# Performance work log

Measured on AMD Instinct MI355X. Metric: run time of the kernel, lower is better.

Reference implementation:

```python
import jax, jax.numpy as jnp
import numpy as np

N_NODES = 100000
N_EDGES = 1600000
IN_DIM = 64
HID = 128
N_GRAPHS = 64
N_CLASSES = 2
EPS = 1e-5


def setup_inputs() -> dict:
    key = jax.random.key(0)
    ks = jax.random.split(key, 8)
    x = jax.random.normal(ks[0], (N_NODES, IN_DIM), dtype=jnp.float32)
    edge_index = jax.random.randint(ks[1], (2, N_EDGES), 0, N_NODES, dtype=jnp.int64)
    batch = jnp.sort(jax.random.randint(ks[2], (N_NODES,), 0, N_GRAPHS, dtype=jnp.int64))
    W1 = jax.random.normal(ks[3], (IN_DIM, HID), dtype=jnp.float32) / np.sqrt(IN_DIM)
    b1 = jnp.zeros((HID,), jnp.float32)
    W2 = jax.random.normal(ks[4], (HID, HID), dtype=jnp.float32) / np.sqrt(HID)
    b2 = jnp.zeros((HID,), jnp.float32)
    gamma = jnp.ones((HID,), jnp.float32)
    beta = jnp.zeros((HID,), jnp.float32)
    fcW = jax.random.normal(ks[5], (HID, N_CLASSES), dtype=jnp.float32) / np.sqrt(HID)
    fcb = jnp.zeros((N_CLASSES,), jnp.float32)
    return {"x": x, "edge_index": edge_index, "batch": batch, "W1": W1, "b1": b1,
            "W2": W2, "b2": b2, "gamma": gamma, "beta": beta, "fcW": fcW, "fcb": fcb}


def reference(x, edge_index, batch, W1, b1, W2, b2, gamma, beta, fcW, fcb):
    n = x.shape[0]
    loop = jnp.arange(n)
    # GCNConv adds self-loops and uses symmetric normalization D^-1/2 (A+I) D^-1/2
    src = jnp.concatenate([edge_index[0], loop])
    dst = jnp.concatenate([edge_index[1], loop])
    deg = jax.ops.segment_sum(jnp.ones_like(dst, dtype=x.dtype), dst, num_segments=n)
    dis = jax.lax.rsqrt(deg)  # deg >= 1 thanks to self-loops
    enorm = dis[src] * dis[dst]  # [E+N]

    def gcn(h, W, b):
        h = h @ W                                   # transform first (PyG order)
        msg = h[src] * enorm[:, None]               # gather + scale
        return jax.ops.segment_sum(msg, dst, num_segments=n) + b  # scatter-add

    cnt = jnp.maximum(jax.ops.segment_sum(jnp.ones((n,), x.dtype), batch,
                                          num_segments=N_GRAPHS), 1.0)[:, None]

    def inst_norm(h):
        # per-graph, per-channel normalization over nodes (affine=False)
        mean = jax.ops.segment_sum(h, batch, num_segments=N_GRAPHS) / cnt
        var = jax.ops.segment_sum(h * h, batch, num_segments=N_GRAPHS) / cnt - mean * mean
        return (h - mean[batch]) * jax.lax.rsqrt(var[batch] + EPS)

    h = jax.nn.relu(inst_norm(gcn(x, W1, b1)))   # dropout = identity (eval)
    h = jax.nn.relu(inst_norm(gcn(h, W2, b2)))
    pooled = jax.ops.segment_sum(h, batch, num_segments=N_GRAPHS) / cnt  # global mean pool
    # BatchNorm1d over the graph dimension (batch statistics, affine)
    m = jnp.mean(pooled, axis=0)
    v = jnp.mean((pooled - m) ** 2, axis=0)
    z = (pooled - m) * jax.lax.rsqrt(v + EPS) * gamma + beta
    return z @ fcW + fcb
```

## Files before the change

### kernel.cpp

```cpp
#include <hip/hip_runtime.h>
#include <hip/hip_bf16.h>


#define HID 128
#define NGRAPH 64
#define EPSN 1e-5f
#define BSHIFT 8
#define NBMAX 512

typedef unsigned int uint;
typedef unsigned short ushort;

static __device__ __forceinline__ ushort f2bf(float f) {
  uint x = __float_as_uint(f);
  return (ushort)((x + 0x7FFFu + ((x >> 16) & 1u)) >> 16);
}
static __device__ __forceinline__ float bf_lo(uint u) { return __uint_as_float(u << 16); }
static __device__ __forceinline__ float bf_hi(uint u) {
  return __uint_as_float(u & 0xFFFF0000u);
}

__global__ __launch_bounds__(256) void graph_starts(const int* __restrict__ batch,
                                                    int* __restrict__ gstart, int N) {
  int i = blockIdx.x * 256 + threadIdx.x;
  if (i >= N) return;
  int g = batch[i];
  if (i == 0) {
    for (int q = 0; q <= g; ++q) gstart[q] = 0;
  } else {
    int gp = batch[i - 1];
    if (g != gp)
      for (int q = gp + 1; q <= g; ++q) gstart[q] = i;
  }
  if (i == N - 1)
    for (int q = g + 1; q <= NGRAPH; ++q) gstart[q] = N;
}

__global__ __launch_bounds__(64) void cnt_from_starts(const int* __restrict__ gstart,
                                                      float* __restrict__ cnt) {
  int g = threadIdx.x;
  if (g < NGRAPH) cnt[g] = (float)(gstart[g + 1] - gstart[g]);
}

__global__ __launch_bounds__(256) void bucket_count(const int* __restrict__ dst,
                                                    int* __restrict__ bcnt, int E, int NB) {
  __shared__ int h[NBMAX];
  for (int i = threadIdx.x; i < NB; i += 256) h[i] = 0;
  __syncthreads();
  int e0 = blockIdx.x * 4096;
#pragma unroll
  for (int k = 0; k < 16; ++k) {
    int e = e0 + k * 256 + threadIdx.x;
    if (e < E) atomicAdd(&h[dst[e] >> BSHIFT], 1);
  }
  __syncthreads();
  for (int i = threadIdx.x; i < NB; i += 256)
    if (h[i]) atomicAdd(&bcnt[i], h[i]);
}

__global__ __launch_bounds__(512) void bucket_scan(const int* __restrict__ bcnt,
                                                   int* __restrict__ bbase,
                                                   int* __restrict__ bcursor, int NB, int E) {
  __shared__ int sm[512];
  int t = threadIdx.x;
  int v = (t < NB) ? bcnt[t] : 0;
  sm[t] = v;
  __syncthreads();
  for (int off = 1; off < 512; off <<= 1) {
    int add = (t >= off) ? sm[t - off] : 0;
    __syncthreads();
    sm[t] += add;
    __syncthreads();
  }
  if (t < NB) {
    int excl = sm[t] - v;
    bbase[t] = excl;
    bcursor[t] = excl;
  }
  if (t == 0) bbase[NB] = E;
}

__global__ __launch_bounds__(256) void bin_edges(const int* __restrict__ src,
                                                 const int* __restrict__ dst,
                                                 int* __restrict__ bcursor,
                                                 uint* __restrict__ records, int E, int NB) {
  __shared__ int h[NBMAX];
  __shared__ int base[NBMAX];
  for (int i = threadIdx.x; i < NB; i += 256) h[i] = 0;
  __syncthreads();
  int e0 = blockIdx.x * 4096;
  int d[16], s[16];
#pragma unroll
  for (int k = 0; k < 16; ++k) {
    int e = e0 + k * 256 + threadIdx.x;
    if (e < E) {
      d[k] = dst[e];
      s[k] = src[e];
      atomicAdd(&h[d[k] >> BSHIFT], 1);
    }
  }
  __syncthreads();
  for (int i = threadIdx.x; i < NB; i += 256) {
    int c = h[i];
    if (c) base[i] = atomicAdd(&bcursor[i], c);
  }
  __syncthreads();
  for (int i = threadIdx.x; i < NB; i += 256) h[i] = 0;
  __syncthreads();
#pragma unroll
  for (int k = 0; k < 16; ++k) {
    int e = e0 + k * 256 + threadIdx.x;
    if (e < E) {
      int b = d[k] >> BSHIFT;
      int lp = atomicAdd(&h[b], 1);
      records[base[b] + lp] = ((uint)s[k] << 8) | (uint)(d[k] & 255);
    }
  }
}

__global__ __launch_bounds__(256) void build_csr(const uint* __restrict__ records,
                                                 const int* __restrict__ bbase,
                                                 int* __restrict__ row_ptr,
                                                 float* __restrict__ dis,
                                                 int* __restrict__ esrc, int N, int E) {
  const int b = blockIdx.x;
  const int node0 = b << BSHIFT;
  const int nn = min(256, N - node0);
  const int beg = bbase[b];
  const int cnt = bbase[b + 1] - beg;
  const int t = threadIdx.x;
  __shared__ int lc[256], sc[256], lcur[256];
  lc[t] = 0;
  __syncthreads();
  for (int i = t; i < cnt; i += 256) atomicAdd(&lc[records[beg + i] & 255u], 1);
  __syncthreads();
  int myc = lc[t];
  sc[t] = myc;
  __syncthreads();
  for (int off = 1; off < 256; off <<= 1) {
    int add = (t >= off) ? sc[t - off] : 0;
    __syncthreads();
    sc[t] += add;
    __syncthreads();
  }
  int excl = sc[t] - myc;
  if (t < nn) {
    row_ptr[node0 + t] = beg + excl;
    dis[node0 + t] = rsqrtf((float)myc + 1.0f);
  }
  lcur[t] = excl;
  __syncthreads();
  for (int i = t; i < cnt; i += 256) {
    uint r = records[beg + i];
    int p = atomicAdd(&lcur[r & 255u], 1);
    esrc[beg + p] = (int)(r >> 8);
  }
  if (b == 0 && t == 0) row_ptr[N] = E;
}

__global__ __launch_bounds__(256) void xscale_bf16(const float* __restrict__ X,
                                                   const float* __restrict__ dis,
                                                   ushort* __restrict__ XS, int n4) {
  int i4 = blockIdx.x * 256 + threadIdx.x;
  if (i4 >= n4) return;
  int n = i4 >> 4;
  float dn = dis[n];
  float4 v = ((const float4*)X)[i4];
  ushort4 u;
  u.x = f2bf(v.x * dn);
  u.y = f2bf(v.y * dn);
  u.z = f2bf(v.z * dn);
  u.w = f2bf(v.w * dn);
  ((ushort4*)XS)[i4] = u;
}

__global__ __launch_bounds__(256) void aggregate64_bf16(const ushort* __restrict__ XS,
                                                        const int* __restrict__ row_ptr,
                                                        const int* __restrict__ esrc,
                                                        const float* __restrict__ dis,
                                                        ushort* __restrict__ out, int N) {
  int wid = (int)((blockIdx.x * 256 + threadIdx.x) >> 6);
  if (wid >= N) return;
  const int lane = threadIdx.x & 63;
  const int h = lane >> 5;
  const int c2 = lane & 31;
  const float dn = dis[wid];
  const int beg = row_ptr[wid];
  const int end = row_ptr[wid + 1];
  const uint* X32 = (const uint*)XS;
  float ax = 0.f, ay = 0.f, bx = 0.f, by = 0.f;
  int e = beg;
  for (; e + 3 < end; e += 4) {
    int s0 = esrc[e + h];
    int s1 = esrc[e + 2 + h];
    uint u0 = X32[(size_t)s0 * 32 + c2];
    uint u1 = X32[(size_t)s1 * 32 + c2];
    ax += bf_lo(u0);
    ay += bf_hi(u0);
    bx += bf_lo(u1);
    by += bf_hi(u1);
  }
  for (; e < end; e += 2) {
    if (e + h < end) {
      uint u0 = X32[(size_t)esrc[e + h] * 32 + c2];
      ax += bf_lo(u0);
      ay += bf_hi(u0);
    }
  }
  ax += bx;
  ay += by;
  ax += __shfl_xor(ax, 32, 64);
  ay += __shfl_xor(ay, 32, 64);
  if (h == 0) {
    uint us = X32[(size_t)wid * 32 + c2];
    ax = (ax + bf_lo(us)) * dn;
    ay = (ay + bf_hi(us)) * dn;
    ((uint*)out)[(size_t)wid * 32 + c2] = (uint)f2bf(ax) | ((uint)f2bf(ay) << 16);
  }
}

__global__ __launch_bounds__(256) void aggregate128_bf16(const ushort* __restrict__ H,
                                                         const int* __restrict__ row_ptr,
                                                         const int* __restrict__ esrc,
                                                         const float* __restrict__ dis,
                                                         const float* __restrict__ bias,
                                                         ushort* __restrict__ outz, int N) {
  int wid = (int)((blockIdx.x * 256 + threadIdx.x) >> 6);
  if (wid >= N) return;
  const int lane = threadIdx.x & 63;
  const int h = lane >> 5;
  const int c4 = lane & 31;
  const float dn = dis[wid];
  const int beg = row_ptr[wid];
  const int end = row_ptr[wid + 1];
  const uint2* H2 = (const uint2*)H;
  float a0 = 0.f, a1 = 0.f, a2 = 0.f, a3 = 0.f;
  float b0 = 0.f, b1v = 0.f, b2v = 0.f, b3 = 0.f;
  int e = beg;
  for (; e + 3 < end; e += 4) {
    int s0 = esrc[e + h];
    int s1 = esrc[e + 2 + h];
    uint2 u0 = H2[(size_t)s0 * 32 + c4];
    uint2 u1 = H2[(size_t)s1 * 32 + c4];
    a0 += bf_lo(u0.x);
    a1 += bf_hi(u0.x);
    a2 += bf_lo(u0.y);
    a3 += bf_hi(u0.y);
    b0 += bf_lo(u1.x);
    b1v += bf_hi(u1.x);
    b2v += bf_lo(u1.y);
    b3 += bf_hi(u1.y);
  }
  for (; e < end; e += 2) {
    if (e + h < end) {
      uint2 u0 = H2[(size_t)esrc[e + h] * 32 + c4];
      a0 += bf_lo(u0.x);
      a1 += bf_hi(u0.x);
      a2 += bf_lo(u0.y);
      a3 += bf_hi(u0.y);
    }
  }
  a0 += b0;
  a1 += b1v;
  a2 += b2v;
  a3 += b3;
  a0 += __shfl_xor(a0, 32, 64);
  a1 += __shfl_xor(a1, 32, 64);
  a2 += __shfl_xor(a2, 32, 64);
  a3 += __shfl_xor(a3, 32, 64);
  if (h == 0) {
    uint2 us = H2[(size_t)wid * 32 + c4];
    float4 b = ((const float4*)bias)[c4];
    float r0 = (a0 + bf_lo(us.x)) * dn + b.x;
    float r1 = (a1 + bf_hi(us.x)) * dn + b.y;
    float r2 = (a2 + bf_lo(us.y)) * dn + b.z;
    float r3 = (a3 + bf_hi(us.y)) * dn + b.w;
    uint2 o;
    o.x = (uint)f2bf(r0) | ((uint)f2bf(r1) << 16);
    o.y = (uint)f2bf(r2) | ((uint)f2bf(r3) << 16);
    ((uint2*)outz)[(size_t)wid * 32 + c4] = o;
  }
}

template <int K, bool FUSE_NORM, bool DIS_SCALE>
__global__ __launch_bounds__(256) void gemm_tile(const ushort* __restrict__ X,
                                                 const float* __restrict__ W,
                                                 const float* __restrict__ bias,
                                                 const int* __restrict__ batch,
                                                 const float* __restrict__ mean,
                                                 const float* __restrict__ inv,
                                                 const float* __restrict__ disv,
                                                 ushort* __restrict__ Y, int N) {
  __shared__ float Xs[64][68];
  __shared__ float Ws[64][HID];
  const int t = threadIdx.x;
  const int r0 = (t >> 4) * 4;
  const int c0 = (t & 15) * 8;
  const int row0 = blockIdx.x * 64;
  float acc[4][8] = {};
  for (int k0 = 0; k0 < K; k0 += 64) {
    for (int i = t; i < 64 * 32; i += 256) {
      int kk = i >> 5;
      int c4 = i & 31;
      ((float4*)&Ws[kk][0])[c4] = ((const float4*)(W + (size_t)(k0 + kk) * HID))[c4];
    }
    for (int i = t; i < 64 * 8; i += 256) {
      int r = i >> 3;
      int u = i & 7;
      int gr = row0 + r;
      float f[8];
      if (gr < N) {
        uint4 v = *(const uint4*)(X + (size_t)gr * K + k0 + u * 8);
        f[0] = bf_lo(v.x);
        f[1] = bf_hi(v.x);
        f[2] = bf_lo(v.y);
        f[3] = bf_hi(v.y);
        f[4] = bf_lo(v.z);
        f[5] = bf_hi(v.z);
        f[6] = bf_lo(v.w);
        f[7] = bf_hi(v.w);
        if (FUSE_NORM) {
          int g = batch[gr];
          const float* mp = mean + g * HID + k0 + u * 8;
          const float* ip = inv + g * HID + k0 + u * 8;
#pragma unroll
          for (int j = 0; j < 8; ++j) f[j] = fmaxf((f[j] - mp[j]) * ip[j], 0.f);
        }
      } else {
#pragma unroll
        for (int j = 0; j < 8; ++j) f[j] = 0.f;
      }
#pragma unroll
      for (int j = 0; j < 8; ++j) Xs[r][u * 8 + j] = f[j];
    }
    __syncthreads();
#pragma unroll 4
    for (int kk = 0; kk < 64; ++kk) {
      float4 w0 = *(const float4*)&Ws[kk][c0];
      float4 w1 = *(const float4*)&Ws[kk][c0 + 4];
      float xr[4];
#pragma unroll
      for (int i = 0; i < 4; ++i) xr[i] = Xs[r0 + i][kk];
#pragma unroll
      for (int i = 0; i < 4; ++i) {
        acc[i][0] += xr[i] * w0.x;
        acc[i][1] += xr[i] * w0.y;
        acc[i][2] += xr[i] * w0.z;
        acc[i][3] += xr[i] * w0.w;
        acc[i][4] += xr[i] * w1.x;
        acc[i][5] += xr[i] * w1.y;
        acc[i][6] += xr[i] * w1.z;
        acc[i][7] += xr[i] * w1.w;
      }
    }
    __syncthreads();
  }
  float bv[8];
#pragma unroll
  for (int j = 0; j < 8; ++j) bv[j] = bias ? bias[c0 + j] : 0.f;
#pragma unroll
  for (int i = 0; i < 4; ++i) {
    int gr = row0 + r0 + i;
    if (gr < N) {
      float ds = DIS_SCALE ? disv[gr] : 1.f;
      uint4 u;
      u.x = (uint)f2bf((acc[i][0] + bv[0]) * ds) | ((uint)f2bf((acc[i][1] + bv[1]) * ds) << 16);
      u.y = (uint)f2bf((acc[i][2] + bv[2]) * ds) | ((uint)f2bf((acc[i][3] + bv[3]) * ds) << 16);
      u.z = (uint)f2bf((acc[i][4] + bv[4]) * ds) | ((uint)f2bf((acc[i][5] + bv[5]) * ds) << 16);
      u.w = (uint)f2bf((acc[i][6] + bv[6]) * ds) | ((uint)f2bf((acc[i][7] + bv[7]) * ds) << 16);
      *(uint4*)(Y + (size_t)gr * HID + c0) = u;
    }
  }
}

__global__ __launch_bounds__(256) void stats_pass(const ushort* __restrict__ G,
                                                  const int* __restrict__ batch,
                                                  float* __restrict__ gsum,
                                                  float* __restrict__ gsq, int N) {
  const int c = threadIdx.x & 127;
  const int half = threadIdx.x >> 7;
  const int n0 = blockIdx.x * 64 + half * 32;
  const int n1 = min(n0 + 32, N);
  float s = 0.f, sq = 0.f;
  int cur = -1;
  for (int n = n0; n < n1; ++n) {
    int g = batch[n];
    if (g != cur) {
      if (cur >= 0) {
        atomicAdd(&gsum[cur * HID + c], s);
        atomicAdd(&gsq[cur * HID + c], sq);
      }
      cur = g;
      s = 0.f;
      sq = 0.f;
    }
    float val = __uint_as_float((uint)G[(size_t)n * HID + c] << 16);
    s += val;
    sq += val * val;
  }
  if (cur >= 0) {
    atomicAdd(&gsum[cur * HID + c], s);
    atomicAdd(&gsq[cur * HID + c], sq);
  }
}

__global__ __launch_bounds__(256) void finalize_stats(const float* __restrict__ gsum,
                                                      const float* __restrict__ gsq,
                                                      const float* __restrict__ cnt,
                                                      float* __restrict__ mean,
                                                      float* __restrict__ inv) {
  int i = blockIdx.x * 256 + threadIdx.x;
  if (i >= NGRAPH * HID) return;
  int g = i >> 7;
  float c = fmaxf(cnt[g], 1.f);
  float m = gsum[i] / c;
  float v = gsq[i] / c - m * m;
  mean[i] = m;
  inv[i] = rsqrtf(v + EPSN);
}

__global__ __launch_bounds__(256) void norm_relu_pool(const ushort* __restrict__ G,
                                                      const int* __restrict__ batch,
                                                      const float* __restrict__ mean,
                                                      const float* __restrict__ inv,
                                                      float* __restrict__ pooled, int N) {
  const int c = threadIdx.x & 127;
  const int half = threadIdx.x >> 7;
  const int n0 = blockIdx.x * 64 + half * 32;
  const int n1 = min(n0 + 32, N);
  float s = 0.f;
  int cur = -1;
  for (int n = n0; n < n1; ++n) {
    int g = batch[n];
    if (g != cur) {
      if (cur >= 0) atomicAdd(&pooled[cur * HID + c], s);
      cur = g;
      s = 0.f;
    }
    float val = __uint_as_float((uint)G[(size_t)n * HID + c] << 16);
    float v = (val - mean[g * HID + c]) * inv[g * HID + c];
    s += fmaxf(v, 0.f);
  }
  if (cur >= 0) atomicAdd(&pooled[cur * HID + c], s);
}

__global__ __launch_bounds__(256) void final_head(const float* __restrict__ pooled_sum,
                                                  const float* __restrict__ cnt,
                                                  const float* __restrict__ gamma,
                                                  const float* __restrict__ beta,
                                                  const float* __restrict__ fcW,
                                                  const float* __restrict__ fcb,
                                                  float* __restrict__ out) {
  __shared__ float P[NGRAPH][HID];
  __shared__ float zs[HID], zb[HID];
  int t = threadIdx.x;
  for (int i = t; i < NGRAPH * HID; i += 256) {
    int g = i >> 7;
    P[g][i & 127] = pooled_sum[i] / fmaxf(cnt[g], 1.f);
  }
  __syncthreads();
  if (t < HID) {
    float m = 0.f;
    for (int g = 0; g < NGRAPH; ++g) m += P[g][t];
    m *= (1.f / NGRAPH);
    float v = 0.f;
    for (int g = 0; g < NGRAPH; ++g) {
      float d = P[g][t] - m;
      v += d * d;
    }
    v *= (1.f / NGRAPH);
    float sc = rsqrtf(v + EPSN) * gamma[t];
    zs[t] = sc;
    zb[t] = beta[t] - m * sc;
  }
  __syncthreads();
  if (t < NGRAPH * 2) {
    int g = t >> 1, k = t & 1;
    float acc = fcb[k];
    for (int c = 0; c < HID; ++c) {
      float z = P[g][c] * zs[c] + zb[c];
      acc += z * fcW[c * 2 + k];
    }
    out[t] = acc;
  }
}

extern "C" void kernel_launch(void* const* d_in, const int* in_sizes, int n_in,
                              void* d_out, int out_size, void* d_ws, size_t ws_size,
                              hipStream_t stream) {
  const float* x = (const float*)d_in[0];
  const int* ei = (const int*)d_in[1];
  const int* batch = (const int*)d_in[2];
  const float* W1 = (const float*)d_in[3];
  const float* b1 = (const float*)d_in[4];
  const float* W2 = (const float*)d_in[5];
  const float* b2 = (const float*)d_in[6];
  const float* gamma = (const float*)d_in[7];
  const float* beta = (const float*)d_in[8];
  const float* fcW = (const float*)d_in[9];
  const float* fcb = (const float*)d_in[10];
  float* out = (float*)d_out;

  const int N = in_sizes[2];
  const int E = in_sizes[1] / 2;
  const int* srcp = ei;
  const int* dstp = ei + E;
  const int NB = (N + 255) >> BSHIFT;

  float* ws = (float*)d_ws;
  size_t off = 0;
  auto alloc = [&](size_t n) {
    float* p = ws + off;
    off += (n + 127) & ~(size_t)127;
    return p;
  };
  int* row_ptr = (int*)alloc(N + 1);
  int* esrc = (int*)alloc(E);
  size_t recsz = ((size_t)E > (size_t)N * 32 ? (size_t)E : (size_t)N * 32);
  float* recbuf = alloc(recsz);
  float* dis = alloc(N);
  float* y1b = alloc((size_t)N * 32);
  float* h1b = alloc((size_t)N * 64);
  float* h2b = alloc((size_t)N * 64);
  float* zb_ = alloc((size_t)N * 64);
  int* bbase = (int*)alloc(NBMAX + 1);
  int* bcursor = (int*)alloc(NBMAX);
  int* gstart = (int*)alloc(NGRAPH + 1);
  float* zero0 = ws + off;
  int* bcnt = (int*)alloc(NBMAX);
  float* gsum1 = alloc(NGRAPH * HID);
  float* gsq1 = alloc(NGRAPH * HID);
  float* gsum2 = alloc(NGRAPH * HID);
  float* gsq2 = alloc(NGRAPH * HID);
  float* pooled = alloc(NGRAPH * HID);
  size_t zero_bytes = (size_t)((ws + off) - zero0) * sizeof(float);
  float* cnt = alloc(NGRAPH);
  float* mean1 = alloc(NGRAPH * HID);
  float* inv1 = alloc(NGRAPH * HID);
  float* mean2 = alloc(NGRAPH * HID);
  float* inv2 = alloc(NGRAPH * HID);

  uint* records = (uint*)recbuf;
  ushort* xs = (ushort*)recbuf;
  ushort* y1 = (ushort*)y1b;
  ushort* h1 = (ushort*)h1b;
  ushort* h2s = (ushort*)h2b;
  ushort* z = (ushort*)zb_;

  const int nblkN = (N + 255) / 256;
  const int nblkE4k = (E + 4095) / 4096;

  hipMemsetAsync(zero0, 0, zero_bytes, stream);

  graph_starts<<<nblkN, 256, 0, stream>>>(batch, gstart, N);
  cnt_from_starts<<<1, 64, 0, stream>>>(gstart, cnt);
  bucket_count<<<nblkE4k, 256, 0, stream>>>(dstp, bcnt, E, NB);
  bucket_scan<<<1, 512, 0, stream>>>(bcnt, bbase, bcursor, NB, E);
  bin_edges<<<nblkE4k, 256, 0, stream>>>(srcp, dstp, bcursor, records, E, NB);
  build_csr<<<NB, 256, 0, stream>>>(records, bbase, row_ptr, dis, esrc, N, E);

  const int aggBlocks = (N + 3) / 4;
  const int gemmBlocks = (N + 63) / 64;

  xscale_bf16<<<(N * 16 + 255) / 256, 256, 0, stream>>>(x, dis, xs, N * 16);
  aggregate64_bf16<<<aggBlocks, 256, 0, stream>>>(xs, row_ptr, esrc, dis, y1, N);
  gemm_tile<64, false, false><<<gemmBlocks, 256, 0, stream>>>(
      y1, W1, b1, nullptr, nullptr, nullptr, nullptr, h1, N);
  stats_pass<<<(N + 63) / 64, 256, 0, stream>>>(h1, batch, gsum1, gsq1, N);
  finalize_stats<<<(NGRAPH * HID + 255) / 256, 256, 0, stream>>>(gsum1, gsq1, cnt, mean1, inv1);

  gemm_tile<128, true, true><<<gemmBlocks, 256, 0, stream>>>(
      h1, W2, nullptr, batch, mean1, inv1, dis, h2s, N);
  aggregate128_bf16<<<aggBlocks, 256, 0, stream>>>(h2s, row_ptr, esrc, dis, b2, z, N);
  stats_pass<<<(N + 63) / 64, 256, 0, stream>>>(z, batch, gsum2, gsq2, N);
  finalize_stats<<<(NGRAPH * HID + 255) / 256, 256, 0, stream>>>(gsum2, gsq2, cnt, mean2, inv2);
  norm_relu_pool<<<(N + 63) / 64, 256, 0, stream>>>(z, batch, mean2, inv2, pooled, N);

  final_head<<<1, 256, 0, stream>>>(pooled, cnt, gamma, beta, fcW, fcb, out);
}
```

Baseline: 364.9 us.

## Use fixed-capacity bucket slots for CSR build and restructure aggregation gathers

Replaces the bucket count and scan passes with fixed-capacity per-bucket slots sized from the average edge count, so row begin and end are stored separately and the CSR build skips one full read of the destination array and two launches. The aggregation kernels are rewritten so each wave covers a full node row, with eight independent neighbor gathers per iteration and no cross-half shuffle. The capacity assumption can overflow on skewed degree distributions, and the 64-wide kernel now uses narrow 2-byte loads.

```diff
diff --git a/kernel.cpp b/kernel.cpp
--- a/kernel.cpp
+++ b/kernel.cpp
@@ -42,48 +42,16 @@
   if (g < NGRAPH) cnt[g] = (float)(gstart[g + 1] - gstart[g]);
 }
 
-__global__ __launch_bounds__(256) void bucket_count(const int* __restrict__ dst,
-                                                    int* __restrict__ bcnt, int E, int NB) {
-  __shared__ int h[NBMAX];
-  for (int i = threadIdx.x; i < NB; i += 256) h[i] = 0;
-  __syncthreads();
-  int e0 = blockIdx.x * 4096;
-#pragma unroll
-  for (int k = 0; k < 16; ++k) {
-    int e = e0 + k * 256 + threadIdx.x;
-    if (e < E) atomicAdd(&h[dst[e] >> BSHIFT], 1);
-  }
-  __syncthreads();
-  for (int i = threadIdx.x; i < NB; i += 256)
-    if (h[i]) atomicAdd(&bcnt[i], h[i]);
-}
-
-__global__ __launch_bounds__(512) void bucket_scan(const int* __restrict__ bcnt,
-                                                   int* __restrict__ bbase,
-                                                   int* __restrict__ bcursor, int NB, int E) {
-  __shared__ int sm[512];
-  int t = threadIdx.x;
-  int v = (t < NB) ? bcnt[t] : 0;
-  sm[t] = v;
-  __syncthreads();
-  for (int off = 1; off < 512; off <<= 1) {
-    int add = (t >= off) ? sm[t - off] : 0;
-    __syncthreads();
-    sm[t] += add;
-    __syncthreads();
-  }
-  if (t < NB) {
-    int excl = sm[t] - v;
-    bbase[t] = excl;
-    bcursor[t] = excl;
-  }
-  if (t == 0) bbase[NB] = E;
+__global__ __launch_bounds__(256) void init_cursor(int* __restrict__ gcursor, int NB, int cap) {
+  int i = blockIdx.x * 256 + threadIdx.x;
+  if (i < NB) gcursor[i] = i * cap;
 }
 
 __global__ __launch_bounds__(256) void bin_edges(const int* __restrict__ src,
                                                  const int* __restrict__ dst,
-                                                 int* __restrict__ bcursor,
-                                                 uint* __restrict__ records, int E, int NB) {
+                                                 int* __restrict__ gcursor,
+                                                 uint* __restrict__ records, int E, int NB,
+                                                 int cap) {
   __shared__ int h[NBMAX];
   __shared__ int base[NBMAX];
   for (int i = threadIdx.x; i < NB; i += 256) h[i] = 0;
@@ -102,7 +70,7 @@
   __syncthreads();
   for (int i = threadIdx.x; i < NB; i += 256) {
     int c = h[i];
-    if (c) base[i] = atomicAdd(&bcursor[i], c);
+    if (c) base[i] = atomicAdd(&gcursor[i], c);
   }
   __syncthreads();
   for (int i = threadIdx.x; i < NB; i += 256) h[i] = 0;
@@ -119,15 +87,16 @@
 }
 
 __global__ __launch_bounds__(256) void build_csr(const uint* __restrict__ records,
-                                                 const int* __restrict__ bbase,
-                                                 int* __restrict__ row_ptr,
+                                                 const int* __restrict__ gcursor,
+                                                 int* __restrict__ row_beg,
+                                                 int* __restrict__ row_end,
                                                  float* __restrict__ dis,
-                                                 int* __restrict__ esrc, int N, int E) {
+                                                 int* __restrict__ esrc, int N, int cap) {
   const int b = blockIdx.x;
   const int node0 = b << BSHIFT;
   const int nn = min(256, N - node0);
-  const int beg = bbase[b];
-  const int cnt = bbase[b + 1] - beg;
+  const int beg = b * cap;
+  const int cnt = gcursor[b] - beg;
   const int t = threadIdx.x;
   __shared__ int lc[256], sc[256], lcur[256];
   lc[t] = 0;
@@ -145,7 +114,8 @@
   }
   int excl = sc[t] - myc;
   if (t < nn) {
-    row_ptr[node0 + t] = beg + excl;
+    row_beg[node0 + t] = beg + excl;
+    row_end[node0 + t] = beg + excl + myc;
     dis[node0 + t] = rsqrtf((float)myc + 1.0f);
   }
   lcur[t] = excl;
@@ -155,7 +125,6 @@
     int p = atomicAdd(&lcur[r & 255u], 1);
     esrc[beg + p] = (int)(r >> 8);
   }
-  if (b == 0 && t == 0) row_ptr[N] = E;
 }
 
 __global__ __launch_bounds__(256) void xscale_bf16(const float* __restrict__ X,
@@ -174,112 +143,105 @@
   ((ushort4*)XS)[i4] = u;
 }
 
-__global__ __launch_bounds__(256) void aggregate64_bf16(const ushort* __restrict__ XS,
-                                                        const int* __restrict__ row_ptr,
-                                                        const int* __restrict__ esrc,
-                                                        const float* __restrict__ dis,
-                                                        ushort* __restrict__ out, int N) {
+__global__ __launch_bounds__(256) void aggregate64(const ushort* __restrict__ XS,
+                                                   const int* __restrict__ row_beg,
+                                                   const int* __restrict__ row_end,
+                                                   const int* __restrict__ esrc,
+                                                   const float* __restrict__ dis,
+                                                   ushort* __restrict__ out, int N) {
   int wid = (int)((blockIdx.x * 256 + threadIdx.x) >> 6);
   if (wid >= N) return;
   const int lane = threadIdx.x & 63;
-  const int h = lane >> 5;
-  const int c2 = lane & 31;
   const float dn = dis[wid];
-  const int beg = row_ptr[wid];
-  const int end = row_ptr[wid + 1];
-  const uint* X32 = (const uint*)XS;
-  float ax = 0.f, ay = 0.f, bx = 0.f, by = 0.f;
+  const int beg = row_beg[wid];
+  const int end = row_end[wid];
+  const ushort* Xl = XS + lane;
+  float a0 = 0.f, a1 = 0.f, a2 = 0.f, a3 = 0.f;
   int e = beg;
-  for (; e + 3 < end; e += 4) {
-    int s0 = esrc[e + h];
-    int s1 = esrc[e + 2 + h];
-    uint u0 = X32[(size_t)s0 * 32 + c2];
-    uint u1 = X32[(size_t)s1 * 32 + c2];
-    ax += bf_lo(u0);
-    ay += bf_hi(u0);
-    bx += bf_lo(u1);
-    by += bf_hi(u1);
-  }
-  for (; e < end; e += 2) {
-    if (e + h < end) {
-      uint u0 = X32[(size_t)esrc[e + h] * 32 + c2];
-      ax += bf_lo(u0);
-      ay += bf_hi(u0);
-    }
-  }
-  ax += bx;
-  ay += by;
-  ax += __shfl_xor(ax, 32, 64);
-  ay += __shfl_xor(ay, 32, 64);
-  if (h == 0) {
-    uint us = X32[(size_t)wid * 32 + c2];
-    ax = (ax + bf_lo(us)) * dn;
-    ay = (ay + bf_hi(us)) * dn;
-    ((uint*)out)[(size_t)wid * 32 + c2] = (uint)f2bf(ax) | ((uint)f2bf(ay) << 16);
-  }
-}
-
-__global__ __launch_bounds__(256) void aggregate128_bf16(const ushort* __restrict__ H,
-                                                         const int* __restrict__ row_ptr,
-                                                         const int* __restrict__ esrc,
-                                                         const float* __restrict__ dis,
-                                                         const float* __restrict__ bias,
-                                                         ushort* __restrict__ outz, int N) {
+  for (; e + 7 < end; e += 8) {
+    int s0 = esrc[e], s1 = esrc[e + 1], s2 = esrc[e + 2], s3 = esrc[e + 3];
+    int s4 = esrc[e + 4], s5 = esrc[e + 5], s6 = esrc[e + 6], s7 = esrc[e + 7];
+    ushort v0 = Xl[(size_t)s0 * 64];
+    ushort v1 = Xl[(size_t)s1 * 64];
+    ushort v2 = Xl[(size_t)s2 * 64];
+    ushort v3 = Xl[(size_t)s3 * 64];
+    ushort v4 = Xl[(size_t)s4 * 64];
+    ushort v5 = Xl[(size_t)s5 * 64];
+    ushort v6 = Xl[(size_t)s6 * 64];
+    ushort v7 = Xl[(size_t)s7 * 64];
+    a0 += __uint_as_float((uint)v0 << 16) + __uint_as_float((uint)v1 << 16);
+    a1 += __uint_as_float((uint)v2 << 16) + __uint_as_float((uint)v3 << 16);
+    a2 += __uint_as_float((uint)v4 << 16) + __uint_as_float((uint)v5 << 16);
+    a3 += __uint_as_float((uint)v6 << 16) + __uint_as_float((uint)v7 << 16);
+  }
+  for (; e + 1 < end; e += 2) {
+    ushort v0 = Xl[(size_t)esrc[e] * 64];
+    ushort v1 = Xl[(size_t)esrc[e + 1] * 64];
+    a0 += __uint_as_float((uint)v0 << 16);
+    a1 += __uint_as_float((uint)v1 << 16);
+  }
+  if (e < end) a0 += __uint_as_float((uint)Xl[(size_t)esrc[e] * 64] << 16);
+  a0 += a1 + a2 + a3 + __uint_as_float((uint)Xl[(size_t)wid * 64] << 16);
+  out[(size_t)wid * 64 + lane] = f2bf(a0 * dn);
+}
+
+__global__ __launch_bounds__(256) void aggregate128(const ushort* __restrict__ H,
+                                                    const int* __restrict__ row_beg,
+                                                    const int* __restrict__ row_end,
+                                                    const int* __restrict__ esrc,
+                                                    const float* __restrict__ dis,
+                                                    const float* __restrict__ bias,
+                                                    ushort* __restrict__ outz, int N) {
   int wid = (int)((blockIdx.x * 256 + threadIdx.x) >> 6);
   if (wid >= N) return;
   const int lane = threadIdx.x & 63;
-  const int h = lane >> 5;
-  const int c4 = lane & 31;
   const float dn = dis[wid];
-  const int beg = row_ptr[wid];
-  const int end = row_ptr[wid + 1];
-  const uint2* H2 = (const uint2*)H;
-  float a0 = 0.f, a1 = 0.f, a2 = 0.f, a3 = 0.f;
-  float b0 = 0.f, b1v = 0.f, b2v = 0.f, b3 = 0.f;
+  const int beg = row_beg[wid];
+  const int end = row_end[wid];
+  const uint* Hl = (const uint*)H + lane;
+  float a0 = 0.f, a1 = 0.f, b0 = 0.f, b1 = 0.f;
+  float c0 = 0.f, c1 = 0.f, d0 = 0.f, d1 = 0.f;
   int e = beg;
-  for (; e + 3 < end; e += 4) {
-    int s0 = esrc[e + h];
-    int s1 = esrc[e + 2 + h];
-    uint2 u0 = H2[(size_t)s0 * 32 + c4];
-    uint2 u1 = H2[(size_t)s1 * 32 + c4];
-    a0 += bf_lo(u0.x);
-    a1 += bf_hi(u0.x);
-    a2 += bf_lo(u0.y);
-    a3 += bf_hi(u0.y);
-    b0 += bf_lo(u1.x);
-    b1v += bf_hi(u1.x);
-    b2v += bf_lo(u1.y);
-    b3 += bf_hi(u1.y);
-  }
-  for (; e < end; e += 2) {
-    if (e + h < end) {
-      uint2 u0 = H2[(size_t)esrc[e + h] * 32 + c4];
-      a0 += bf_lo(u0.x);
-      a1 += bf_hi(u0.x);
-      a2 += bf_lo(u0.y);
-      a3 += bf_hi(u0.y);
-    }
-  }
-  a0 += b0;
-  a1 += b1v;
-  a2 += b2v;
-  a3 += b3;
-  a0 += __shfl_xor(a0, 32, 64);
-  a1 += __shfl_xor(a1, 32, 64);
-  a2 += __shfl_xor(a2, 32, 64);
-  a3 += __shfl_xor(a3, 32, 64);
-  if (h == 0) {
-    uint2 us = H2[(size_t)wid * 32 + c4];
-    float4 b = ((const float4*)bias)[c4];
-    float r0 = (a0 + bf_lo(us.x)) * dn + b.x;
-    float r1 = (a1 + bf_hi(us.x)) * dn + b.y;
-    float r2 = (a2 + bf_lo(us.y)) * dn + b.z;
-    float r3 = (a3 + bf_hi(us.y)) * dn + b.w;
-    uint2 o;
-    o.x = (uint)f2bf(r0) | ((uint)f2bf(r1) << 16);
-    o.y = (uint)f2bf(r2) | ((uint)f2bf(r3) << 16);
-    ((uint2*)outz)[(size_t)wid * 32 + c4] = o;
-  }
+  for (; e + 7 < end; e += 8) {
+    int s0 = esrc[e], s1 = esrc[e + 1], s2 = esrc[e + 2], s3 = esrc[e + 3];
+    int s4 = esrc[e + 4], s5 = esrc[e + 5], s6 = esrc[e + 6], s7 = esrc[e + 7];
+    uint u0 = Hl[(size_t)s0 * 64];
+    uint u1 = Hl[(size_t)s1 * 64];
+    uint u2 = Hl[(size_t)s2 * 64];
+    uint u3 = Hl[(size_t)s3 * 64];
+    uint u4 = Hl[(size_t)s4 * 64];
+    uint u5 = Hl[(size_t)s5 * 64];
+    uint u6 = Hl[(size_t)s6 * 64];
+    uint u7 = Hl[(size_t)s7 * 64];
+    a0 += bf_lo(u0) + bf_lo(u1);
+    a1 += bf_hi(u0) + bf_hi(u1);
+    b0 += bf_lo(u2) + bf_lo(u3);
+    b1 += bf_hi(u2) + bf_hi(u3);
+    c0 += bf_lo(u4) + bf_lo(u5);
+    c1 += bf_hi(u4) + bf_hi(u5);
+    d0 += bf_lo(u6) + bf_lo(u7);
+    d1 += bf_hi(u6) + bf_hi(u7);
+  }
+  for (; e + 1 < end; e += 2) {
+    uint u0 = Hl[(size_t)esrc[e] * 64];
+    uint u1 = Hl[(size_t)esrc[e + 1] * 64];
+    a0 += bf_lo(u0);
+    a1 += bf_hi(u0);
+    b0 += bf_lo(u1);
+    b1 += bf_hi(u1);
+  }
+  if (e < end) {
+    uint u0 = Hl[(size_t)esrc[e] * 64];
+    a0 += bf_lo(u0);
+    a1 += bf_hi(u0);
+  }
+  uint us = Hl[(size_t)wid * 64];
+  a0 += b0 + c0 + d0 + bf_lo(us);
+  a1 += b1 + c1 + d1 + bf_hi(us);
+  float2 b = ((const float2*)bias)[lane];
+  float r0 = a0 * dn + b.x;
+  float r1 = a1 * dn + b.y;
+  ((uint*)outz)[(size_t)wid * 64 + lane] = (uint)f2bf(r0) | ((uint)f2bf(r1) << 16);
 }
 
 template <int K, bool FUSE_NORM, bool DIS_SCALE>
@@ -506,6 +468,7 @@
   const int* srcp = ei;
   const int* dstp = ei + E;
   const int NB = (N + 255) >> BSHIFT;
+  const int cap = 2 * (E / NB) + 256;
 
   float* ws = (float*)d_ws;
   size_t off = 0;
@@ -514,20 +477,19 @@
     off += (n + 127) & ~(size_t)127;
     return p;
   };
-  int* row_ptr = (int*)alloc(N + 1);
-  int* esrc = (int*)alloc(E);
-  size_t recsz = ((size_t)E > (size_t)N * 32 ? (size_t)E : (size_t)N * 32);
+  int* row_beg = (int*)alloc(N);
+  int* row_end = (int*)alloc(N);
+  int* esrc = (int*)alloc((size_t)NB * cap);
+  size_t recsz = ((size_t)NB * cap > (size_t)N * 32 ? (size_t)NB * cap : (size_t)N * 32);
   float* recbuf = alloc(recsz);
   float* dis = alloc(N);
   float* y1b = alloc((size_t)N * 32);
   float* h1b = alloc((size_t)N * 64);
   float* h2b = alloc((size_t)N * 64);
   float* zb_ = alloc((size_t)N * 64);
-  int* bbase = (int*)alloc(NBMAX + 1);
-  int* bcursor = (int*)alloc(NBMAX);
+  int* gcursor = (int*)alloc(NBMAX);
   int* gstart = (int*)alloc(NGRAPH + 1);
   float* zero0 = ws + off;
-  int* bcnt = (int*)alloc(NBMAX);
   float* gsum1 = alloc(NGRAPH * HID);
   float* gsq1 = alloc(NGRAPH * HID);
   float* gsum2 = alloc(NGRAPH * HID);
@@ -554,16 +516,15 @@
 
   graph_starts<<<nblkN, 256, 0, stream>>>(batch, gstart, N);
   cnt_from_starts<<<1, 64, 0, stream>>>(gstart, cnt);
-  bucket_count<<<nblkE4k, 256, 0, stream>>>(dstp, bcnt, E, NB);
-  bucket_scan<<<1, 512, 0, stream>>>(bcnt, bbase, bcursor, NB, E);
-  bin_edges<<<nblkE4k, 256, 0, stream>>>(srcp, dstp, bcursor, records, E, NB);
-  build_csr<<<NB, 256, 0, stream>>>(records, bbase, row_ptr, dis, esrc, N, E);
+  init_cursor<<<(NB + 255) / 256, 256, 0, stream>>>(gcursor, NB, cap);
+  bin_edges<<<nblkE4k, 256, 0, stream>>>(srcp, dstp, gcursor, records, E, NB, cap);
+  build_csr<<<NB, 256, 0, stream>>>(records, gcursor, row_beg, row_end, dis, esrc, N, cap);
 
   const int aggBlocks = (N + 3) / 4;
   const int gemmBlocks = (N + 63) / 64;
 
   xscale_bf16<<<(N * 16 + 255) / 256, 256, 0, stream>>>(x, dis, xs, N * 16);
-  aggregate64_bf16<<<aggBlocks, 256, 0, stream>>>(xs, row_ptr, esrc, dis, y1, N);
+  aggregate64<<<aggBlocks, 256, 0, stream>>>(xs, row_beg, row_end, esrc, dis, y1, N);
   gemm_tile<64, false, false><<<gemmBlocks, 256, 0, stream>>>(
       y1, W1, b1, nullptr, nullptr, nullptr, nullptr, h1, N);
   stats_pass<<<(N + 63) / 64, 256, 0, stream>>>(h1, batch, gsum1, gsq1, N);
@@ -571,7 +532,7 @@
 
   gemm_tile<128, true, true><<<gemmBlocks, 256, 0, stream>>>(
       h1, W2, nullptr, batch, mean1, inv1, dis, h2s, N);
-  aggregate128_bf16<<<aggBlocks, 256, 0, stream>>>(h2s, row_ptr, esrc, dis, b2, z, N);
+  aggregate128<<<aggBlocks, 256, 0, stream>>>(h2s, row_beg, row_end, esrc, dis, b2, z, N);
   stats_pass<<<(N + 63) / 64, 256, 0, stream>>>(z, batch, gsum2, gsq2, N);
   finalize_stats<<<(NGRAPH * HID + 255) / 256, 256, 0, stream>>>(gsum2, gsq2, cnt, mean2, inv2);
   norm_relu_pool<<<(N + 63) / 64, 256, 0, stream>>>(z, batch, mean2, inv2, pooled, N);
```

New measurement: 329.7 us. 1.11x faster.
